# Performance work log

Hardware: AMD Instinct MI355X
Metric: run time of the kernel (lower is better)

## Reference

```python
import jax, jax.numpy as jnp
import numpy as np

B, T, D_IN, H, D_OUT = 256, 512, 64, 256, 8


def setup_inputs() -> dict:
    key = jax.random.key(0)
    ks = jax.random.split(key, 6)
    s_ih = 1.0 / np.sqrt(H)
    inputs = jax.random.normal(ks[0], (B, T, D_IN), dtype=jnp.float32)
    h0 = jnp.zeros((B, H), dtype=jnp.float32)
    c0 = jnp.zeros((B, H), dtype=jnp.float32)
    # LSTM cell params, PyTorch gate order (i, f, g, o)
    W_ih = jax.random.uniform(ks[1], (4 * H, D_IN), minval=-s_ih, maxval=s_ih, dtype=jnp.float32)
    W_hh = jax.random.uniform(ks[2], (4 * H, H), minval=-s_ih, maxval=s_ih, dtype=jnp.float32)
    b = jax.random.uniform(ks[3], (4 * H,), minval=-s_ih, maxval=s_ih, dtype=jnp.float32)
    # output projection (xavier_uniform weight, zero bias)
    lim = np.sqrt(6.0 / (H + D_OUT))
    W_out = jax.random.uniform(ks[4], (D_OUT, H), minval=-lim, maxval=lim, dtype=jnp.float32)
    b_out = jnp.zeros((D_OUT,), dtype=jnp.float32)
    return {"inputs": inputs, "h0": h0, "c0": c0, "W_ih": W_ih, "W_hh": W_hh,
            "b": b, "W_out": W_out, "b_out": b_out}


def _lstm_last(inputs, h0, c0, W_ih, W_hh, b):
    # inputs: [B, T, D_in] -> scan over time, keep only final hidden state
    xs = jnp.swapaxes(inputs, 0, 1)  # [T, B, D_in]

    def step(carry, x_t):
        h, c = carry
        gates = x_t @ W_ih.T + h @ W_hh.T + b  # [B, 4H]
        i, f, g, o = jnp.split(gates, 4, axis=-1)
        c_new = jax.nn.sigmoid(f) * c + jax.nn.sigmoid(i) * jnp.tanh(g)
        h_new = jax.nn.sigmoid(o) * jnp.tanh(c_new)
        return (h_new, c_new), None

    (h, c), _ = jax.lax.scan(step, (h0, c0), xs)
    return h, c


def reference(inputs, h0, c0, W_ih, W_hh, b, W_out, b_out):
    h, c = _lstm_last(inputs, h0, c0, W_ih, W_hh, b)
    rnn_outputs = h  # last-timestep output (dropout_prob=0 -> identity)
    logits = rnn_outputs @ W_out.T + b_out
    return (rnn_outputs, logits, h, c)
```

## Files before the change

### kernel.cpp

```cpp
#include <hip/hip_runtime.h>

#define T_ 512
#define B_ 256
#define H_ 256
#define DIN_ 64

typedef __attribute__((ext_vector_type(8))) short short8;
typedef __attribute__((ext_vector_type(4))) float f32x4;
typedef __attribute__((ext_vector_type(4))) unsigned int u32x4;

__device__ __forceinline__ unsigned short f2bf(float f) {
  unsigned u = __float_as_uint(f);
  u += 0x7FFFu + ((u >> 16) & 1u);
  return (unsigned short)(u >> 16);
}
__device__ __forceinline__ float bf2f(unsigned short s) {
  return __uint_as_float(((unsigned)s) << 16);
}
__device__ __forceinline__ float sigm(float x) { return 1.0f / (1.0f + __expf(-x)); }
__device__ __forceinline__ float tanh_(float x) {
  float xx = fminf(fmaxf(x, -30.0f), 30.0f);
  float e = __expf(2.0f * xx);
  return (e - 1.0f) / (e + 1.0f);
}

__device__ __forceinline__ void load16_sc1(const unsigned* p, u32x4& a,
                                           u32x4& b, u32x4& c, u32x4& d) {
  asm volatile(
      "global_load_dwordx4 %0, %4, off sc1\n\t"
      "global_load_dwordx4 %1, %4, off offset:16 sc1\n\t"
      "global_load_dwordx4 %2, %4, off offset:32 sc1\n\t"
      "global_load_dwordx4 %3, %4, off offset:48 sc1\n\t"
      "s_waitcnt vmcnt(0)"
      : "=v"(a), "=v"(b), "=v"(c), "=v"(d)
      : "v"(p) : "memory");
}

__device__ __forceinline__ bool tags_ok(u32x4 a, u32x4 b, u32x4 c, u32x4 d,
                                        unsigned w) {
  unsigned m = (a.x >> 16) ^ w; m |= (a.y >> 16) ^ w;
  m |= (a.z >> 16) ^ w;         m |= (a.w >> 16) ^ w;
  m |= (b.x >> 16) ^ w;         m |= (b.y >> 16) ^ w;
  m |= (b.z >> 16) ^ w;         m |= (b.w >> 16) ^ w;
  m |= (c.x >> 16) ^ w;         m |= (c.y >> 16) ^ w;
  m |= (c.z >> 16) ^ w;         m |= (c.w >> 16) ^ w;
  m |= (d.x >> 16) ^ w;         m |= (d.y >> 16) ^ w;
  m |= (d.z >> 16) ^ w;         m |= (d.w >> 16) ^ w;
  return m == 0;
}

__global__ __launch_bounds__(256) void lstm_kern(
    const float* __restrict__ xin, const float* __restrict__ h0f,
    const float* __restrict__ c0f, const float* __restrict__ Wih,
    const float* __restrict__ Whh, const float* __restrict__ bias,
    const float* __restrict__ Wout, const float* __restrict__ bout,
    float* __restrict__ out, unsigned* hbuf32)
{
  const int tid = threadIdx.x;
  const int gb  = blockIdx.x >> 4;
  const int gc  = blockIdx.x & 15;
  const int wv  = tid >> 6;
  const int ln  = tid & 63;
  const int colB = ln & 15;
  const int krow = ln >> 4;

  __shared__ unsigned short h_s[16 * 264];
  __shared__ unsigned short x_s[16 * 72];
  __shared__ float gbuf[4 * 16 * 17];

  const int j = wv * H_ + gc * 16 + colB;
  short8 bh[8], bx[2];
  #pragma unroll
  for (int kc = 0; kc < 8; ++kc) {
    const float* p = Whh + j * H_ + kc * 32 + krow * 8;
    short8 f;
    #pragma unroll
    for (int i = 0; i < 8; ++i) f[i] = (short)f2bf(p[i]);
    bh[kc] = f;
  }
  #pragma unroll
  for (int kc = 0; kc < 2; ++kc) {
    const float* p = Wih + j * DIN_ + kc * 32 + krow * 8;
    short8 f;
    #pragma unroll
    for (int i = 0; i < 8; ++i) f[i] = (short)f2bf(p[i]);
    bx[kc] = f;
  }
  const float bval = bias[j];

  const int er = tid >> 4, ec = tid & 15;
  const int grow = gb * 16 + er;
  float c_val = c0f[grow * H_ + gc * 16 + ec];
  float h_val = 0.0f;

  const int hr = tid >> 4;
  const int hcb = (tid & 15) * 16;
  const unsigned* ldp_base = hbuf32 + gb * 4096 + hr * 256 + hcb;
  unsigned* stp_base = hbuf32 + gb * 4096 + er * 256 + gc * 16 + ec;

  for (int s = 1; s <= T_; ++s) {
    {
      int r = tid >> 4, d4 = (tid & 15) * 4;
      float4 v = *(const float4*)(xin + ((gb * 16 + r) * T_ + (s - 1)) * DIN_ + d4);
      unsigned short* q = &x_s[r * 72 + d4];
      q[0] = f2bf(v.x); q[1] = f2bf(v.y); q[2] = f2bf(v.z); q[3] = f2bf(v.w);
    }

    if (s == 1) {
      #pragma unroll
      for (int it = 0; it < 4; ++it) {
        int e4 = tid + it * 256;
        int r = e4 >> 6, c4 = e4 & 63;
        const float4* p = (const float4*)(h0f + (gb * 16 + r) * H_) + c4;
        float4 v = *p;
        unsigned short* q = &h_s[r * 264 + c4 * 4];
        q[0] = f2bf(v.x); q[1] = f2bf(v.y); q[2] = f2bf(v.z); q[3] = f2bf(v.w);
      }
    } else {
      const unsigned want = (unsigned)(s - 1);
      const unsigned* ldp = ldp_base + (((s - 1) & 1) << 16);
      u32x4 va, vb, vc, vd;
      int tries = 0;
      do {
        load16_sc1(ldp, va, vb, vc, vd);
        if (tags_ok(va, vb, vc, vd, want)) break;
      } while (++tries < (1 << 18));
      unsigned* q32 = (unsigned*)&h_s[hr * 264 + hcb];
      q32[0] = (va.x & 0xFFFFu) | (va.y << 16);
      q32[1] = (va.z & 0xFFFFu) | (va.w << 16);
      q32[2] = (vb.x & 0xFFFFu) | (vb.y << 16);
      q32[3] = (vb.z & 0xFFFFu) | (vb.w << 16);
      q32[4] = (vc.x & 0xFFFFu) | (vc.y << 16);
      q32[5] = (vc.z & 0xFFFFu) | (vc.w << 16);
      q32[6] = (vd.x & 0xFFFFu) | (vd.y << 16);
      q32[7] = (vd.z & 0xFFFFu) | (vd.w << 16);
    }
    __syncthreads();

    f32x4 acc = {0.f, 0.f, 0.f, 0.f};
    #pragma unroll
    for (int kc = 0; kc < 2; ++kc) {
      short8 a = *(const short8*)&x_s[colB * 72 + kc * 32 + krow * 8];
      acc = __builtin_amdgcn_mfma_f32_16x16x32_bf16(a, bx[kc], acc, 0, 0, 0);
    }
    #pragma unroll
    for (int kc = 0; kc < 8; ++kc) {
      short8 a = *(const short8*)&h_s[colB * 264 + kc * 32 + krow * 8];
      acc = __builtin_amdgcn_mfma_f32_16x16x32_bf16(a, bh[kc], acc, 0, 0, 0);
    }
    #pragma unroll
    for (int i = 0; i < 4; ++i)
      gbuf[wv * 272 + (krow * 4 + i) * 17 + colB] = acc[i] + bval;
    __syncthreads();

    float gi = gbuf[0 * 272 + er * 17 + ec];
    float gf = gbuf[1 * 272 + er * 17 + ec];
    float gg = gbuf[2 * 272 + er * 17 + ec];
    float go = gbuf[3 * 272 + er * 17 + ec];
    c_val = sigm(gf) * c_val + sigm(gi) * tanh_(gg);
    h_val = sigm(go) * tanh_(c_val);

    unsigned pk = ((unsigned)s << 16) | (unsigned)f2bf(h_val);
    __hip_atomic_store(stp_base + ((s & 1) << 16), pk,
                       __ATOMIC_RELAXED, __HIP_MEMORY_SCOPE_AGENT);
  }

  const int gj = gc * 16 + ec;
  out[grow * H_ + gj] = h_val;
  out[67584 + grow * H_ + gj] = h_val;
  out[133120 + grow * H_ + gj] = c_val;

  if (gc == 0) {
    const unsigned want = (unsigned)T_;
    const unsigned* ldp = ldp_base + ((T_ & 1) << 16);
    u32x4 va, vb, vc, vd;
    int tries = 0;
    do {
      load16_sc1(ldp, va, vb, vc, vd);
      if (tags_ok(va, vb, vc, vd, want)) break;
    } while (++tries < (1 << 18));
    unsigned* q32 = (unsigned*)&h_s[hr * 264 + hcb];
    q32[0] = (va.x & 0xFFFFu) | (va.y << 16);
    q32[1] = (va.z & 0xFFFFu) | (va.w << 16);
    q32[2] = (vb.x & 0xFFFFu) | (vb.y << 16);
    q32[3] = (vb.z & 0xFFFFu) | (vb.w << 16);
    q32[4] = (vc.x & 0xFFFFu) | (vc.y << 16);
    q32[5] = (vc.z & 0xFFFFu) | (vc.w << 16);
    q32[6] = (vd.x & 0xFFFFu) | (vd.y << 16);
    q32[7] = (vd.z & 0xFFFFu) | (vd.w << 16);
    __syncthreads();
    if (tid < 128) {
      int r = tid >> 3, o = tid & 7;
      float a = bout[o];
      for (int k = 0; k < H_; ++k)
        a = fmaf(bf2f(h_s[r * 264 + k]), Wout[o * H_ + k], a);
      out[65536 + (gb * 16 + r) * 8 + o] = a;
    }
  }
}

extern "C" void kernel_launch(void* const* d_in, const int* in_sizes, int n_in,
                              void* d_out, int out_size, void* d_ws, size_t ws_size,
                              hipStream_t stream) {
  const float* xin  = (const float*)d_in[0];
  const float* h0f  = (const float*)d_in[1];
  const float* c0f  = (const float*)d_in[2];
  const float* Wih  = (const float*)d_in[3];
  const float* Whh  = (const float*)d_in[4];
  const float* bias = (const float*)d_in[5];
  const float* Wout = (const float*)d_in[6];
  const float* bout = (const float*)d_in[7];
  float* out = (float*)d_out;

  unsigned* hbuf32 = (unsigned*)d_ws;

  void* args[] = {&xin, &h0f, &c0f, &Wih, &Whh, &bias, &Wout, &bout,
                  &out, &hbuf32};
  hipLaunchCooperativeKernel((void*)lstm_kern, dim3(256), dim3(256),
                             args, 0, stream);
}
```

Baseline: 1.176 ms.

## Interleave gate columns per wave and exchange gates via shuffles, double-buffer LDS

New measurement: 1.214 ms. 1.03x slower.

```diff
diff --git a/kernel.cpp b/kernel.cpp
--- a/kernel.cpp
+++ b/kernel.cpp
@@ -64,11 +64,11 @@
   const int colB = ln & 15;
   const int krow = ln >> 4;
 
-  __shared__ unsigned short h_s[16 * 264];
-  __shared__ unsigned short x_s[16 * 72];
-  __shared__ float gbuf[4 * 16 * 17];
-
-  const int j = wv * H_ + gc * 16 + colB;
+  __shared__ unsigned short h_s[2][16 * 264];
+  __shared__ unsigned short x_s[2][16 * 72];
+
+  const int gg = colB >> 2, qq = colB & 3;
+  const int j = gg * H_ + gc * 16 + wv * 4 + qq;
   short8 bh[8], bx[2];
   #pragma unroll
   for (int kc = 0; kc < 8; ++kc) {
@@ -88,33 +88,37 @@
   }
   const float bval = bias[j];
 
-  const int er = tid >> 4, ec = tid & 15;
-  const int grow = gb * 16 + er;
-  float c_val = c0f[grow * H_ + gc * 16 + ec];
+  const int quad = ln >> 4;
+  const int r_lo = (ln >> 2) & 3;
+  const int q    = ln & 3;
+  const int erow = quad * 4 + r_lo;
+  const int grow = gb * 16 + erow;
+  const int gcol = gc * 16 + wv * 4 + q;
+  float c_val = c0f[grow * H_ + gcol];
   float h_val = 0.0f;
 
   const int hr = tid >> 4;
   const int hcb = (tid & 15) * 16;
   const unsigned* ldp_base = hbuf32 + gb * 4096 + hr * 256 + hcb;
-  unsigned* stp_base = hbuf32 + gb * 4096 + er * 256 + gc * 16 + ec;
+  unsigned* stp_base = hbuf32 + gb * 4096 + erow * 256 + gcol;
+
+  const float* xrow = xin + ((gb * 16 + (tid >> 4)) * T_) * DIN_ + (tid & 15) * 4;
 
   for (int s = 1; s <= T_; ++s) {
+    const int p = (s - 1) & 1;
     {
-      int r = tid >> 4, d4 = (tid & 15) * 4;
-      float4 v = *(const float4*)(xin + ((gb * 16 + r) * T_ + (s - 1)) * DIN_ + d4);
-      unsigned short* q = &x_s[r * 72 + d4];
-      q[0] = f2bf(v.x); q[1] = f2bf(v.y); q[2] = f2bf(v.z); q[3] = f2bf(v.w);
-    }
-
+      float4 v = *(const float4*)(xrow + (s - 1) * DIN_);
+      unsigned short* qp = &x_s[p][(tid >> 4) * 72 + (tid & 15) * 4];
+      qp[0] = f2bf(v.x); qp[1] = f2bf(v.y); qp[2] = f2bf(v.z); qp[3] = f2bf(v.w);
+    }
     if (s == 1) {
       #pragma unroll
       for (int it = 0; it < 4; ++it) {
         int e4 = tid + it * 256;
         int r = e4 >> 6, c4 = e4 & 63;
-        const float4* p = (const float4*)(h0f + (gb * 16 + r) * H_) + c4;
-        float4 v = *p;
-        unsigned short* q = &h_s[r * 264 + c4 * 4];
-        q[0] = f2bf(v.x); q[1] = f2bf(v.y); q[2] = f2bf(v.z); q[3] = f2bf(v.w);
+        float4 v = *((const float4*)(h0f + (gb * 16 + r) * H_) + c4);
+        unsigned short* qp = &h_s[p][r * 264 + c4 * 4];
+        qp[0] = f2bf(v.x); qp[1] = f2bf(v.y); qp[2] = f2bf(v.z); qp[3] = f2bf(v.w);
       }
     } else {
       const unsigned want = (unsigned)(s - 1);
@@ -125,7 +129,7 @@
         load16_sc1(ldp, va, vb, vc, vd);
         if (tags_ok(va, vb, vc, vd, want)) break;
       } while (++tries < (1 << 18));
-      unsigned* q32 = (unsigned*)&h_s[hr * 264 + hcb];
+      unsigned* q32 = (unsigned*)&h_s[p][hr * 264 + hcb];
       q32[0] = (va.x & 0xFFFFu) | (va.y << 16);
       q32[1] = (va.z & 0xFFFFu) | (va.w << 16);
       q32[2] = (vb.x & 0xFFFFu) | (vb.y << 16);
@@ -140,35 +144,40 @@
     f32x4 acc = {0.f, 0.f, 0.f, 0.f};
     #pragma unroll
     for (int kc = 0; kc < 2; ++kc) {
-      short8 a = *(const short8*)&x_s[colB * 72 + kc * 32 + krow * 8];
+      short8 a = *(const short8*)&x_s[p][colB * 72 + kc * 32 + krow * 8];
       acc = __builtin_amdgcn_mfma_f32_16x16x32_bf16(a, bx[kc], acc, 0, 0, 0);
     }
     #pragma unroll
     for (int kc = 0; kc < 8; ++kc) {
-      short8 a = *(const short8*)&h_s[colB * 264 + kc * 32 + krow * 8];
+      short8 a = *(const short8*)&h_s[p][colB * 264 + kc * 32 + krow * 8];
       acc = __builtin_amdgcn_mfma_f32_16x16x32_bf16(a, bh[kc], acc, 0, 0, 0);
     }
-    #pragma unroll
-    for (int i = 0; i < 4; ++i)
-      gbuf[wv * 272 + (krow * 4 + i) * 17 + colB] = acc[i] + bval;
-    __syncthreads();
-
-    float gi = gbuf[0 * 272 + er * 17 + ec];
-    float gf = gbuf[1 * 272 + er * 17 + ec];
-    float gg = gbuf[2 * 272 + er * 17 + ec];
-    float go = gbuf[3 * 272 + er * 17 + ec];
-    c_val = sigm(gf) * c_val + sigm(gi) * tanh_(gg);
-    h_val = sigm(go) * tanh_(c_val);
-
+
+    float v0 = acc[0] + bval, v1 = acc[1] + bval,
+          v2 = acc[2] + bval, v3 = acc[3] + bval;
+    {
+      int g0 = (ln >> 2) & 1;
+      float s0 = g0 ? v0 : v1, s1 = g0 ? v2 : v3;
+      float t0 = __shfl_xor(s0, 4, 64), t1 = __shfl_xor(s1, 4, 64);
+      if (g0) { v0 = t0; v2 = t1; } else { v1 = t0; v3 = t1; }
+    }
+    {
+      int g1 = (ln >> 3) & 1;
+      float s0 = g1 ? v0 : v2, s1 = g1 ? v1 : v3;
+      float t0 = __shfl_xor(s0, 8, 64), t1 = __shfl_xor(s1, 8, 64);
+      if (g1) { v0 = t0; v1 = t1; } else { v2 = t0; v3 = t1; }
+    }
+
+    c_val = sigm(v1) * c_val + sigm(v0) * tanh_(v2);
+    h_val = sigm(v3) * tanh_(c_val);
     unsigned pk = ((unsigned)s << 16) | (unsigned)f2bf(h_val);
     __hip_atomic_store(stp_base + ((s & 1) << 16), pk,
                        __ATOMIC_RELAXED, __HIP_MEMORY_SCOPE_AGENT);
   }
 
-  const int gj = gc * 16 + ec;
-  out[grow * H_ + gj] = h_val;
-  out[67584 + grow * H_ + gj] = h_val;
-  out[133120 + grow * H_ + gj] = c_val;
+  out[grow * H_ + gcol] = h_val;
+  out[67584 + grow * H_ + gcol] = h_val;
+  out[133120 + grow * H_ + gcol] = c_val;
 
   if (gc == 0) {
     const unsigned want = (unsigned)T_;
@@ -179,7 +188,7 @@
       load16_sc1(ldp, va, vb, vc, vd);
       if (tags_ok(va, vb, vc, vd, want)) break;
     } while (++tries < (1 << 18));
-    unsigned* q32 = (unsigned*)&h_s[hr * 264 + hcb];
+    unsigned* q32 = (unsigned*)&h_s[0][hr * 264 + hcb];
     q32[0] = (va.x & 0xFFFFu) | (va.y << 16);
     q32[1] = (va.z & 0xFFFFu) | (va.w << 16);
     q32[2] = (vb.x & 0xFFFFu) | (vb.y << 16);
@@ -193,7 +202,7 @@
       int r = tid >> 3, o = tid & 7;
       float a = bout[o];
       for (int k = 0; k < H_; ++k)
-        a = fmaf(bf2f(h_s[r * 264 + k]), Wout[o * H_ + k], a);
+        a = fmaf(bf2f(h_s[0][r * 264 + k]), Wout[o * H_ + k], a);
       out[65536 + (gb * 16 + r) * 8 + o] = a;
     }
   }
```
